# Optimization experiments

Hardware: AMD Instinct MI355X
Metric: run time of the kernel (lower is better)

The kernel has to match this reference:

```python
import jax, jax.numpy as jnp
import numpy as np

VOCAB, VDIM, DDIM, BATCH = 50257, 300, 512, 16


def setup_inputs() -> dict:
    key = jax.random.key(0)
    k1, k2, k3, k4, k5 = jax.random.split(key, 5)
    return {
        "decoder_hidden": jax.random.normal(k1, (BATCH, DDIM), dtype=jnp.float32),
        "embedding_vocab": jax.random.normal(k2, (VOCAB, VDIM), dtype=jnp.float32),
        "W_dec": jax.random.normal(k3, (VDIM, DDIM), dtype=jnp.float32) * (1.0 / np.sqrt(DDIM)),
        "b_dec": jax.random.normal(k4, (VDIM,), dtype=jnp.float32) * 0.01,
        "W_full": jax.random.normal(k5, (VDIM,), dtype=jnp.float32) * (1.0 / np.sqrt(VDIM)),
        "b_full": jnp.zeros((), dtype=jnp.float32),
    }


def reference(decoder_hidden, embedding_vocab, W_dec, b_dec, W_full, b_full):
    # query: (B, vocab_dim) = decoder_att(decoder_hidden)
    query = decoder_hidden @ W_dec.T + b_dec
    # additive scores: relu(vocab + query) projected to scalar -> (B, V)
    hidden = jax.nn.relu(embedding_vocab[None, :, :] + query[:, None, :])  # (B, V, D)
    att = jnp.einsum("bvd,d->bv", hidden, W_full) + b_full
    alpha = jax.nn.softmax(att, axis=1)  # softmax over vocab
    # weighted sum of vocab embeddings: (B, vocab_dim)
    attention_weighted_encoding = jnp.einsum("bv,vd->bd", alpha, embedding_vocab)
    return attention_weighted_encoding, alpha
```

## Files before the change

### kernel.cpp

```cpp
#include <hip/hip_runtime.h>

constexpr int V  = 50257;
constexpr int D  = 300;
constexpr int KD = 512;
constexpr int B  = 16;

constexpr int NB_ATT = (V + 63) / 64;
constexpr int NC  = 512;
constexpr int RPC = (V + NC - 1) / NC;

constexpr float NEG_HUGE = -1.0e30f;

constexpr size_t WS_QT   = 0;
constexpr size_t WS_STAT = 4800;
constexpr size_t WS_MS   = WS_STAT + (size_t)NB_ATT * 32;
constexpr size_t WS_PART = WS_MS + 32;
constexpr size_t WS_TMP  = WS_PART + (size_t)NC * 4800;

struct f4 { float v[4]; };
__device__ __forceinline__ f4 ld4(const float* p) {
    float4 t = *(const float4*)p;
    return {t.x, t.y, t.z, t.w};
}

__global__ void __launch_bounds__(256) k_query(
    const float* __restrict__ dh, const float* __restrict__ Wdec,
    const float* __restrict__ bdec, float* __restrict__ q_t)
{
    int wid  = (blockIdx.x * 256 + threadIdx.x) >> 6;
    int lane = threadIdx.x & 63;
    if (wid >= D * B) return;
    int d = wid >> 4, b = wid & 15;
    const float* wrow = Wdec + (size_t)d * KD;
    const float* hrow = dh + (size_t)b * KD;
    float s = 0.f;
    for (int k = lane; k < KD; k += 64) s += wrow[k] * hrow[k];
    #pragma unroll
    for (int off = 32; off; off >>= 1) s += __shfl_down(s, off, 64);
    if (lane == 0) q_t[d * 16 + b] = s + bdec[d];
}

__global__ void __launch_bounds__(256) k_att(
    const float* __restrict__ E, const float* __restrict__ q_t,
    const float* __restrict__ wf, const float* __restrict__ bf,
    float* __restrict__ att, float* __restrict__ blkstats)
{
    __shared__ float sq[4800];
    __shared__ float sw[304];
    int t = threadIdx.x;
    for (int i = t; i < 4800; i += 256) {
        int d = i >> 4, b = i & 15;
        int bq = b >> 2, bl = b & 3;
        int col = (bq + (d >> 2)) & 3;
        sq[(d << 4) + (col << 2) + bl] = q_t[i];
    }
    for (int i = t; i < 304; i += 256) sw[i] = (i < 300) ? wf[i] : 0.f;
    __syncthreads();

    const int bg   = t >> 6;
    const int lane = t & 63;
    const int rs   = lane >> 2;
    const int p    = lane & 3;
    const int p4   = p << 2;
    const int rot4 = ((bg + p) & 3) << 2;
    const int v0   = blockIdx.x << 6;

    const float* ep[4];
    bool rvalid[4];
    #pragma unroll
    for (int j = 0; j < 4; ++j) {
        int row = v0 + rs + (j << 4);
        rvalid[j] = row < V;
        ep[j] = E + (size_t)(rvalid[j] ? row : (V - 1)) * D;
    }

    float acc[4][4];
    #pragma unroll
    for (int j = 0; j < 4; ++j)
        #pragma unroll
        for (int b = 0; b < 4; ++b) acc[j][b] = 0.f;

    f4 ec[4], en[4];
    #pragma unroll
    for (int j = 0; j < 4; ++j) ec[j] = ld4(ep[j] + p4);

    for (int k = 0; k < 19; ++k) {
        int d0 = (k << 4) + p4;
        bool cur_ok = d0 < D;
        int dn = d0 + 16;
        int dns = (dn < D) ? dn : p4;
        #pragma unroll
        for (int j = 0; j < 4; ++j) en[j] = ld4(ep[j] + dns);
        if (cur_ok) {
            f4 wv = ld4(sw + d0);
            #pragma unroll
            for (int i = 0; i < 4; ++i) {
                f4 qv = ld4(sq + ((d0 + i) << 4) + rot4);
                float wi = wv.v[i];
                #pragma unroll
                for (int j = 0; j < 4; ++j) {
                    float e = ec[j].v[i];
                    #pragma unroll
                    for (int b = 0; b < 4; ++b)
                        acc[j][b] = fmaf(fmaxf(e + qv.v[b], 0.f), wi, acc[j][b]);
                }
            }
        }
        #pragma unroll
        for (int j = 0; j < 4; ++j) ec[j] = en[j];
    }

    #pragma unroll
    for (int j = 0; j < 4; ++j)
        #pragma unroll
        for (int b = 0; b < 4; ++b) {
            float s = acc[j][b];
            s += __shfl_xor(s, 1, 64);
            s += __shfl_xor(s, 2, 64);
            acc[j][b] = s;
        }

    float bfull = bf[0];
    float vj[4];
    float m_l = NEG_HUGE;
    #pragma unroll
    for (int j = 0; j < 4; ++j) {
        float s = (p == 0) ? acc[j][0] : (p == 1) ? acc[j][1]
                : (p == 2) ? acc[j][2] : acc[j][3];
        s += bfull;
        int row = v0 + rs + (j << 4);
        if (rvalid[j]) att[(size_t)((bg << 2) + p) * V + row] = s;
        vj[j] = rvalid[j] ? s : NEG_HUGE;
        m_l = fmaxf(m_l, vj[j]);
    }
    float s_l = 0.f;
    #pragma unroll
    for (int j = 0; j < 4; ++j) s_l += __expf(vj[j] - m_l);

    #pragma unroll
    for (int sh = 2; sh < 6; ++sh) {
        int mask = 1 << sh;
        float mo = __shfl_xor(m_l, mask, 64);
        float so = __shfl_xor(s_l, mask, 64);
        float mn = fmaxf(m_l, mo);
        s_l = s_l * __expf(m_l - mn) + so * __expf(mo - mn);
        m_l = mn;
    }
    if (rs == 0) {
        size_t idx = ((size_t)blockIdx.x * 16 + (bg << 2) + p) * 2;
        blkstats[idx]     = m_l;
        blkstats[idx + 1] = s_l;
    }
}

__global__ void __launch_bounds__(64) k_combine(
    const float* __restrict__ blkstats, float* __restrict__ MS)
{
    int b = blockIdx.x, lane = threadIdx.x;
    float m = NEG_HUGE;
    for (int c = lane; c < NB_ATT; c += 64)
        m = fmaxf(m, blkstats[(size_t)(c * 16 + b) * 2]);
    #pragma unroll
    for (int off = 32; off; off >>= 1) m = fmaxf(m, __shfl_xor(m, off, 64));
    float s = 0.f;
    for (int c = lane; c < NB_ATT; c += 64)
        s += blkstats[(size_t)(c * 16 + b) * 2 + 1] *
             __expf(blkstats[(size_t)(c * 16 + b) * 2] - m);
    #pragma unroll
    for (int off = 32; off; off >>= 1) s += __shfl_xor(s, off, 64);
    if (lane == 0) { MS[b * 2] = m; MS[b * 2 + 1] = 1.f / s; }
}

__global__ void __launch_bounds__(256) k_alpha(
    float* __restrict__ att, const float* __restrict__ MS)
{
    int b = blockIdx.y;
    int v = blockIdx.x * 256 + threadIdx.x;
    if (v >= V) return;
    float M = MS[b * 2], invS = MS[b * 2 + 1];
    size_t i = (size_t)b * V + v;
    att[i] = __expf(att[i] - M) * invS;
}

__global__ void __launch_bounds__(320) k_wsum(
    const float* __restrict__ E, const float* __restrict__ alpha,
    float* __restrict__ partials)
{
    int c = blockIdx.x, t = threadIdx.x;
    if (t >= D) return;
    int v0 = c * RPC, v1 = min(v0 + RPC, V);
    float acc[16];
    #pragma unroll
    for (int b = 0; b < 16; ++b) acc[b] = 0.f;
    int v = v0;
    for (; v + 4 <= v1; v += 4) {
        float e0 = E[(size_t)v * D + t];
        float e1 = E[(size_t)(v + 1) * D + t];
        float e2 = E[(size_t)(v + 2) * D + t];
        float e3 = E[(size_t)(v + 3) * D + t];
        #pragma unroll
        for (int b = 0; b < 16; ++b) {
            const float* ap = alpha + (size_t)b * V + v;
            float a0 = ap[0], a1 = ap[1], a2 = ap[2], a3 = ap[3];
            acc[b] = fmaf(a0, e0, acc[b]);
            acc[b] = fmaf(a1, e1, acc[b]);
            acc[b] = fmaf(a2, e2, acc[b]);
            acc[b] = fmaf(a3, e3, acc[b]);
        }
    }
    for (; v < v1; ++v) {
        float e = E[(size_t)v * D + t];
        #pragma unroll
        for (int b = 0; b < 16; ++b)
            acc[b] = fmaf(alpha[(size_t)b * V + v], e, acc[b]);
    }
    #pragma unroll
    for (int b = 0; b < 16; ++b)
        partials[(size_t)c * 4800 + b * D + t] = acc[b];
}

__global__ void __launch_bounds__(256) k_red1(
    const float* __restrict__ partials, float* __restrict__ tmp)
{
    int o = blockIdx.x * 256 + threadIdx.x;
    if (o >= 4800) return;
    int y = blockIdx.y;
    float s = 0.f;
    for (int c = y * 32; c < y * 32 + 32; ++c)
        s += partials[(size_t)c * 4800 + o];
    tmp[(size_t)y * 4800 + o] = s;
}

__global__ void __launch_bounds__(256) k_red2(
    const float* __restrict__ tmp, float* __restrict__ out)
{
    int o = blockIdx.x * 256 + threadIdx.x;
    if (o >= 4800) return;
    float s = 0.f;
    #pragma unroll
    for (int y = 0; y < 16; ++y) s += tmp[(size_t)y * 4800 + o];
    out[o] = s;
}

extern "C" void kernel_launch(void* const* d_in, const int* in_sizes, int n_in,
                              void* d_out, int out_size, void* d_ws, size_t ws_size,
                              hipStream_t stream) {
    const float* dh   = (const float*)d_in[0];
    const float* E    = (const float*)d_in[1];
    const float* Wdec = (const float*)d_in[2];
    const float* bdec = (const float*)d_in[3];
    const float* wf   = (const float*)d_in[4];
    const float* bf   = (const float*)d_in[5];
    float* out = (float*)d_out;
    float* ws  = (float*)d_ws;

    float* q_t   = ws + WS_QT;
    float* stats = ws + WS_STAT;
    float* MS    = ws + WS_MS;
    float* part  = ws + WS_PART;
    float* tmp   = ws + WS_TMP;
    float* att   = out + 4800;

    k_query<<<(D * B + 3) / 4, 256, 0, stream>>>(dh, Wdec, bdec, q_t);
    k_att<<<NB_ATT, 256, 0, stream>>>(E, q_t, wf, bf, att, stats);
    k_combine<<<B, 64, 0, stream>>>(stats, MS);
    k_alpha<<<dim3((V + 255) / 256, B), 256, 0, stream>>>(att, MS);
    k_wsum<<<NC, 320, 0, stream>>>(E, att, part);
    k_red1<<<dim3(19, 16), 256, 0, stream>>>(part, tmp);
    k_red2<<<19, 256, 0, stream>>>(tmp, out);
}
```

Baseline: 85.44 us.

## Halve rows per attention block, vectorize loads, unroll weighted-sum loop wider

The attention-score kernel now handles 32 vocab rows per block instead of 64, which doubles the block count and adds an occupancy hint to launch_bounds. The query staging into shared memory, and both partial-sum reduction kernels, now use float4 loads and stores. The weighted-sum loop is unrolled 8 rows at a time instead of 4. Together these aim to improve parallelism and latency hiding, in exchange for twice as many per-block stats entries, more shared-memory staging overhead per row, and higher register pressure in the weighted-sum loop.

```diff
diff --git a/kernel.cpp b/kernel.cpp
--- a/kernel.cpp
+++ b/kernel.cpp
@@ -5,7 +5,8 @@
 constexpr int KD = 512;
 constexpr int B  = 16;
 
-constexpr int NB_ATT = (V + 63) / 64;
+constexpr int ROWS = 32;
+constexpr int NB_ATT = (V + ROWS - 1) / ROWS;
 constexpr int NC  = 512;
 constexpr int RPC = (V + NC - 1) / NC;
 
@@ -40,7 +41,7 @@
     if (lane == 0) q_t[d * 16 + b] = s + bdec[d];
 }
 
-__global__ void __launch_bounds__(256) k_att(
+__global__ void __launch_bounds__(256, 6) k_att(
     const float* __restrict__ E, const float* __restrict__ q_t,
     const float* __restrict__ wf, const float* __restrict__ bf,
     float* __restrict__ att, float* __restrict__ blkstats)
@@ -48,11 +49,11 @@
     __shared__ float sq[4800];
     __shared__ float sw[304];
     int t = threadIdx.x;
-    for (int i = t; i < 4800; i += 256) {
-        int d = i >> 4, b = i & 15;
-        int bq = b >> 2, bl = b & 3;
+    for (int i4 = t * 4; i4 < 4800; i4 += 1024) {
+        float4 qv = *(const float4*)(q_t + i4);
+        int d = i4 >> 4, bq = (i4 & 15) >> 2;
         int col = (bq + (d >> 2)) & 3;
-        sq[(d << 4) + (col << 2) + bl] = q_t[i];
+        *(float4*)(sq + (d << 4) + (col << 2)) = qv;
     }
     for (int i = t; i < 304; i += 256) sw[i] = (i < 300) ? wf[i] : 0.f;
     __syncthreads();
@@ -63,26 +64,26 @@
     const int p    = lane & 3;
     const int p4   = p << 2;
     const int rot4 = ((bg + p) & 3) << 2;
-    const int v0   = blockIdx.x << 6;
-
-    const float* ep[4];
-    bool rvalid[4];
-    #pragma unroll
-    for (int j = 0; j < 4; ++j) {
+    const int v0   = blockIdx.x << 5;
+
+    const float* ep[2];
+    bool rvalid[2];
+    #pragma unroll
+    for (int j = 0; j < 2; ++j) {
         int row = v0 + rs + (j << 4);
         rvalid[j] = row < V;
         ep[j] = E + (size_t)(rvalid[j] ? row : (V - 1)) * D;
     }
 
-    float acc[4][4];
-    #pragma unroll
-    for (int j = 0; j < 4; ++j)
+    float acc[2][4];
+    #pragma unroll
+    for (int j = 0; j < 2; ++j)
         #pragma unroll
         for (int b = 0; b < 4; ++b) acc[j][b] = 0.f;
 
-    f4 ec[4], en[4];
-    #pragma unroll
-    for (int j = 0; j < 4; ++j) ec[j] = ld4(ep[j] + p4);
+    f4 ec[2], en[2];
+    #pragma unroll
+    for (int j = 0; j < 2; ++j) ec[j] = ld4(ep[j] + p4);
 
     for (int k = 0; k < 19; ++k) {
         int d0 = (k << 4) + p4;
@@ -90,7 +91,7 @@
         int dn = d0 + 16;
         int dns = (dn < D) ? dn : p4;
         #pragma unroll
-        for (int j = 0; j < 4; ++j) en[j] = ld4(ep[j] + dns);
+        for (int j = 0; j < 2; ++j) en[j] = ld4(ep[j] + dns);
         if (cur_ok) {
             f4 wv = ld4(sw + d0);
             #pragma unroll
@@ -98,7 +99,7 @@
                 f4 qv = ld4(sq + ((d0 + i) << 4) + rot4);
                 float wi = wv.v[i];
                 #pragma unroll
-                for (int j = 0; j < 4; ++j) {
+                for (int j = 0; j < 2; ++j) {
                     float e = ec[j].v[i];
                     #pragma unroll
                     for (int b = 0; b < 4; ++b)
@@ -107,11 +108,11 @@
             }
         }
         #pragma unroll
-        for (int j = 0; j < 4; ++j) ec[j] = en[j];
-    }
-
-    #pragma unroll
-    for (int j = 0; j < 4; ++j)
+        for (int j = 0; j < 2; ++j) ec[j] = en[j];
+    }
+
+    #pragma unroll
+    for (int j = 0; j < 2; ++j)
         #pragma unroll
         for (int b = 0; b < 4; ++b) {
             float s = acc[j][b];
@@ -121,10 +122,10 @@
         }
 
     float bfull = bf[0];
-    float vj[4];
+    float vj[2];
     float m_l = NEG_HUGE;
     #pragma unroll
-    for (int j = 0; j < 4; ++j) {
+    for (int j = 0; j < 2; ++j) {
         float s = (p == 0) ? acc[j][0] : (p == 1) ? acc[j][1]
                 : (p == 2) ? acc[j][2] : acc[j][3];
         s += bfull;
@@ -133,9 +134,7 @@
         vj[j] = rvalid[j] ? s : NEG_HUGE;
         m_l = fmaxf(m_l, vj[j]);
     }
-    float s_l = 0.f;
-    #pragma unroll
-    for (int j = 0; j < 4; ++j) s_l += __expf(vj[j] - m_l);
+    float s_l = __expf(vj[0] - m_l) + __expf(vj[1] - m_l);
 
     #pragma unroll
     for (int sh = 2; sh < 6; ++sh) {
@@ -193,19 +192,17 @@
     #pragma unroll
     for (int b = 0; b < 16; ++b) acc[b] = 0.f;
     int v = v0;
-    for (; v + 4 <= v1; v += 4) {
-        float e0 = E[(size_t)v * D + t];
-        float e1 = E[(size_t)(v + 1) * D + t];
-        float e2 = E[(size_t)(v + 2) * D + t];
-        float e3 = E[(size_t)(v + 3) * D + t];
+    for (; v + 8 <= v1; v += 8) {
+        float e[8];
+        #pragma unroll
+        for (int r = 0; r < 8; ++r) e[r] = E[(size_t)(v + r) * D + t];
         #pragma unroll
         for (int b = 0; b < 16; ++b) {
             const float* ap = alpha + (size_t)b * V + v;
-            float a0 = ap[0], a1 = ap[1], a2 = ap[2], a3 = ap[3];
-            acc[b] = fmaf(a0, e0, acc[b]);
-            acc[b] = fmaf(a1, e1, acc[b]);
-            acc[b] = fmaf(a2, e2, acc[b]);
-            acc[b] = fmaf(a3, e3, acc[b]);
+            float a = acc[b];
+            #pragma unroll
+            for (int r = 0; r < 8; ++r) a = fmaf(ap[r], e[r], a);
+            acc[b] = a;
         }
     }
     for (; v < v1; ++v) {
@@ -222,24 +219,29 @@
 __global__ void __launch_bounds__(256) k_red1(
     const float* __restrict__ partials, float* __restrict__ tmp)
 {
-    int o = blockIdx.x * 256 + threadIdx.x;
-    if (o >= 4800) return;
+    int o4 = blockIdx.x * 256 + threadIdx.x;
+    if (o4 >= 1200) return;
     int y = blockIdx.y;
-    float s = 0.f;
-    for (int c = y * 32; c < y * 32 + 32; ++c)
-        s += partials[(size_t)c * 4800 + o];
-    tmp[(size_t)y * 4800 + o] = s;
+    float4 s = {0.f, 0.f, 0.f, 0.f};
+    for (int c = y * 32; c < y * 32 + 32; ++c) {
+        float4 p = *(const float4*)(partials + (size_t)c * 4800 + o4 * 4);
+        s.x += p.x; s.y += p.y; s.z += p.z; s.w += p.w;
+    }
+    *(float4*)(tmp + (size_t)y * 4800 + o4 * 4) = s;
 }
 
 __global__ void __launch_bounds__(256) k_red2(
     const float* __restrict__ tmp, float* __restrict__ out)
 {
-    int o = blockIdx.x * 256 + threadIdx.x;
-    if (o >= 4800) return;
-    float s = 0.f;
-    #pragma unroll
-    for (int y = 0; y < 16; ++y) s += tmp[(size_t)y * 4800 + o];
-    out[o] = s;
+    int o4 = blockIdx.x * 256 + threadIdx.x;
+    if (o4 >= 1200) return;
+    float4 s = {0.f, 0.f, 0.f, 0.f};
+    #pragma unroll
+    for (int y = 0; y < 16; ++y) {
+        float4 p = *(const float4*)(tmp + (size_t)y * 4800 + o4 * 4);
+        s.x += p.x; s.y += p.y; s.z += p.z; s.w += p.w;
+    }
+    *(float4*)(out + o4 * 4) = s;
 }
 
 extern "C" void kernel_launch(void* const* d_in, const int* in_sizes, int n_in,
@@ -266,6 +268,6 @@
     k_combine<<<B, 64, 0, stream>>>(stats, MS);
     k_alpha<<<dim3((V + 255) / 256, B), 256, 0, stream>>>(att, MS);
     k_wsum<<<NC, 320, 0, stream>>>(E, att, part);
-    k_red1<<<dim3(19, 16), 256, 0, stream>>>(part, tmp);
-    k_red2<<<19, 256, 0, stream>>>(tmp, out);
-}
+    k_red1<<<dim3(5, 16), 256, 0, stream>>>(part, tmp);
+    k_red2<<<5, 256, 0, stream>>>(tmp, out);
+}
```

Measured after the change: 84.81 us. Within noise of the previous version (-0.7%).
